# Optimization experiments

Measured on AMD Instinct MI355X. Metric: run time of the kernel, lower is better.

The kernel has to match this reference:

```python
import jax, jax.numpy as jnp
import numpy as np

N_NODES = 100000
N_EDGES = 3200000
F_IN, F_HID, F_OUT = 512, 16, 64


def gcn_conv(x, src, dst, W, b, n):
    # Linear transform first (PyG GCNConv: x @ W, then normalized aggregation, then + bias)
    xw = x @ W  # [n, f_out]
    # symmetric normalization with self-loops (gcn_norm, improved=False)
    deg = jax.ops.segment_sum(jnp.ones_like(dst, dtype=xw.dtype), dst, num_segments=n)
    deg_inv_sqrt = jnp.where(deg > 0, jax.lax.rsqrt(jnp.maximum(deg, 1e-12)), 0.0)
    norm = deg_inv_sqrt[src] * deg_inv_sqrt[dst]  # [E+n]
    out = jax.ops.segment_sum(norm[:, None] * xw[src], dst, num_segments=n)
    return out + b


def setup_inputs() -> dict:
    key = jax.random.key(0)
    k1, k2, k3, k4, k5, k6 = jax.random.split(key, 6)
    x = jax.random.normal(k1, (N_NODES, F_IN), dtype=jnp.float32)
    edge_index = jax.random.randint(k2, (2, N_EDGES), 0, N_NODES, dtype=jnp.int64)
    # Glorot init like PyG GCNConv
    s1 = (6.0 / (F_IN + F_HID)) ** 0.5
    s2 = (6.0 / (F_HID + F_OUT)) ** 0.5
    W1 = jax.random.uniform(k3, (F_IN, F_HID), jnp.float32, -s1, s1)
    b1 = jnp.zeros((F_HID,), jnp.float32)
    W2 = jax.random.uniform(k4, (F_HID, F_OUT), jnp.float32, -s2, s2)
    b2 = jnp.zeros((F_OUT,), jnp.float32)
    return {"x": x, "edge_index": edge_index, "W1": W1, "b1": b1, "W2": W2, "b2": b2}


def reference(x, edge_index, W1, b1, W2, b2):
    n = x.shape[0]
    loop = jnp.arange(n, dtype=edge_index.dtype)
    src = jnp.concatenate([edge_index[0], loop])
    dst = jnp.concatenate([edge_index[1], loop])
    h = jax.nn.relu(gcn_conv(x, src, dst, W1, b1, n))
    out = jax.nn.relu(gcn_conv(h, src, dst, W2, b2, n))
    return out
```

## Files before the change

### kernel.cpp

```cpp
#include <hip/hip_runtime.h>

constexpr int NN   = 100000;
constexpr int NE   = 3200000;
constexpr int FIN  = 512;
constexpr int FH   = 16;
constexpr int FOUT = 64;

constexpr int BSH = 6;
constexpr int BSZ = 64;
constexpr int K   = (NN + BSZ - 1) / BSZ;
constexpr int NB  = 512;
constexpr int CHUNK = NE / NB;
constexpr int CAP = 4096;

constexpr int G1B = 1024;
constexpr int G1T = 128;
constexpr int NPB = 98;

__global__ __launch_bounds__(256) void k_cnt(const int* __restrict__ ei, int* __restrict__ M) {
    __shared__ int h[K];
    int t = threadIdx.x, b = blockIdx.x;
    for (int i = t; i < K; i += 256) h[i] = 0;
    __syncthreads();
    int e0 = b * CHUNK, eend = e0 + CHUNK;
    int e = e0 + 4 * t;
    for (; e + 4 <= eend; e += 1024) {
        int d0 = ei[NE + e],     d1 = ei[NE + e + 1];
        int d2 = ei[NE + e + 2], d3 = ei[NE + e + 3];
        atomicAdd(&h[d0 >> BSH], 1);
        atomicAdd(&h[d1 >> BSH], 1);
        atomicAdd(&h[d2 >> BSH], 1);
        atomicAdd(&h[d3 >> BSH], 1);
    }
    for (int ee = e; ee < eend && ee < e + 4; ++ee)
        atomicAdd(&h[ei[NE + ee] >> BSH], 1);
    __syncthreads();
    for (int i = t; i < K; i += 256) M[i * NB + b] = h[i];
}

__global__ __launch_bounds__(256) void k_scanM(int* __restrict__ M, int* __restrict__ btot) {
    int k = blockIdx.x, t = threadIdx.x;
    int2* row = (int2*)(M + (size_t)k * NB);
    int2 v = row[t];
    int s = v.x + v.y;
    int lane = t & 63, wid = t >> 6;
    int ps = s;
    #pragma unroll
    for (int off = 1; off < 64; off <<= 1) {
        int u = __shfl_up(ps, off, 64);
        if (lane >= off) ps += u;
    }
    __shared__ int wsum[4];
    if (lane == 63) wsum[wid] = ps;
    __syncthreads();
    int base = 0;
    for (int w = 0; w < wid; ++w) base += wsum[w];
    int excl = base + ps - s;
    int2 o; o.x = excl; o.y = excl + v.x;
    row[t] = o;
    if (t == 255) btot[k] = excl + s;
}

__global__ __launch_bounds__(1024) void k_scanB(const int* __restrict__ btot, int* __restrict__ bstart) {
    int t = threadIdx.x;
    int i0 = 2 * t, i1 = 2 * t + 1;
    int c0 = (i0 < K) ? btot[i0] : 0;
    int c1 = (i1 < K) ? btot[i1] : 0;
    int s = c0 + c1;
    int lane = t & 63, wid = t >> 6;
    int ps = s;
    #pragma unroll
    for (int off = 1; off < 64; off <<= 1) {
        int u = __shfl_up(ps, off, 64);
        if (lane >= off) ps += u;
    }
    __shared__ int wsum[16];
    if (lane == 63) wsum[wid] = ps;
    __syncthreads();
    int base = 0;
    for (int w = 0; w < wid; ++w) base += wsum[w];
    int excl = base + ps - s;
    if (i0 < K) bstart[i0] = excl;
    if (i1 < K) bstart[i1] = excl + c0;
    if (t == 0) bstart[K] = NE;
}

__global__ __launch_bounds__(256) void k_scatter2(const int* __restrict__ ei,
                                                  const int* __restrict__ M,
                                                  const int* __restrict__ bstart,
                                                  int* __restrict__ rec) {
    __shared__ int cur[K];
    int t = threadIdx.x, b = blockIdx.x;
    for (int i = t; i < K; i += 256) cur[i] = bstart[i] + M[i * NB + b];
    __syncthreads();
    int e0 = b * CHUNK, eend = e0 + CHUNK;
    int e = e0 + 4 * t;
    for (; e + 4 <= eend; e += 1024) {
        int s0 = ei[e],     s1 = ei[e + 1],     s2 = ei[e + 2],     s3 = ei[e + 3];
        int d0 = ei[NE + e], d1 = ei[NE + e + 1], d2 = ei[NE + e + 2], d3 = ei[NE + e + 3];
        int p0 = atomicAdd(&cur[d0 >> BSH], 1);
        int p1 = atomicAdd(&cur[d1 >> BSH], 1);
        int p2 = atomicAdd(&cur[d2 >> BSH], 1);
        int p3 = atomicAdd(&cur[d3 >> BSH], 1);
        rec[p0] = (s0 << BSH) | (d0 & (BSZ - 1));
        rec[p1] = (s1 << BSH) | (d1 & (BSZ - 1));
        rec[p2] = (s2 << BSH) | (d2 & (BSZ - 1));
        rec[p3] = (s3 << BSH) | (d3 & (BSZ - 1));
    }
    for (int ee = e; ee < eend && ee < e + 4; ++ee) {
        int s = ei[ee];
        int d = ei[NE + ee];
        int pos = atomicAdd(&cur[d >> BSH], 1);
        rec[pos] = (s << BSH) | (d & (BSZ - 1));
    }
}

__global__ __launch_bounds__(256) void k_sort2(const int* __restrict__ rec1,
                                               const int* __restrict__ bstart,
                                               int* __restrict__ rec2,
                                               int* __restrict__ row_ptr,
                                               float* __restrict__ dis) {
    __shared__ int h[BSZ];
    __shared__ int cur[BSZ];
    int t = threadIdx.x, k = blockIdx.x;
    if (t < BSZ) h[t] = 0;
    __syncthreads();
    int e0 = bstart[k], e1 = bstart[k + 1];
    {
        int e = e0 + 4 * t;
        for (; e + 4 <= e1; e += 1024) {
            int r0 = rec1[e], r1 = rec1[e + 1], r2 = rec1[e + 2], r3 = rec1[e + 3];
            atomicAdd(&h[r0 & (BSZ - 1)], 1);
            atomicAdd(&h[r1 & (BSZ - 1)], 1);
            atomicAdd(&h[r2 & (BSZ - 1)], 1);
            atomicAdd(&h[r3 & (BSZ - 1)], 1);
        }
        for (int ee = e; ee < e1 && ee < e + 4; ++ee)
            atomicAdd(&h[rec1[ee] & (BSZ - 1)], 1);
    }
    __syncthreads();
    if (t < BSZ) {
        int c = h[t];
        int ps = c;
        #pragma unroll
        for (int off = 1; off < 64; off <<= 1) {
            int u = __shfl_up(ps, off, 64);
            if (t >= off) ps += u;
        }
        int excl = ps - c;
        cur[t] = excl;
        int node = k * BSZ + t;
        if (node < NN) {
            row_ptr[node] = e0 + excl;
            dis[node] = rsqrtf((float)c + 1.0f);
        }
    }
    __syncthreads();
    {
        int e = e0 + 4 * t;
        for (; e + 4 <= e1; e += 1024) {
            int r0 = rec1[e], r1 = rec1[e + 1], r2 = rec1[e + 2], r3 = rec1[e + 3];
            int p0 = atomicAdd(&cur[r0 & (BSZ - 1)], 1);
            int p1 = atomicAdd(&cur[r1 & (BSZ - 1)], 1);
            int p2 = atomicAdd(&cur[r2 & (BSZ - 1)], 1);
            int p3 = atomicAdd(&cur[r3 & (BSZ - 1)], 1);
            rec2[e0 + p0] = r0 >> BSH;
            rec2[e0 + p1] = r1 >> BSH;
            rec2[e0 + p2] = r2 >> BSH;
            rec2[e0 + p3] = r3 >> BSH;
        }
        for (int ee = e; ee < e1 && ee < e + 4; ++ee) {
            int r = rec1[ee];
            int pos = atomicAdd(&cur[r & (BSZ - 1)], 1);
            rec2[e0 + pos] = r >> BSH;
        }
    }
    if (k == 0 && t == 0) row_ptr[NN] = NE;
}

__device__ __forceinline__ void cons16(float acc[FH], float4 a0, float4 a1, float4 a2, float4 a3,
                                       const float* __restrict__ wrow) {
    float xs[16] = {a0.x, a0.y, a0.z, a0.w, a1.x, a1.y, a1.z, a1.w,
                    a2.x, a2.y, a2.z, a2.w, a3.x, a3.y, a3.z, a3.w};
    #pragma unroll
    for (int c = 0; c < 16; ++c) {
        float xv = xs[c];
        const float* w = &wrow[c * FH];
        #pragma unroll
        for (int jb = 0; jb < 4; ++jb) {
            float4 wv = *(const float4*)&w[jb * 4];
            acc[jb * 4 + 0] += xv * wv.x;
            acc[jb * 4 + 1] += xv * wv.y;
            acc[jb * 4 + 2] += xv * wv.z;
            acc[jb * 4 + 3] += xv * wv.w;
        }
    }
}

__global__ __launch_bounds__(G1T) void k_gemm1(const float* __restrict__ x,
                                               const float* __restrict__ W1,
                                               const float* __restrict__ dis,
                                               float* __restrict__ vp1) {
    __shared__ float ws[FIN * FH];
    int t = threadIdx.x;
    #pragma unroll
    for (int i = 0; i < 16; ++i)
        *(float4*)&ws[i * 512 + t * 4] = *(const float4*)&W1[i * 512 + t * 4];
    int node = blockIdx.x * NPB + t;
    bool live = (t < NPB) && (node < NN);
    int n = live ? node : NN - 1;
    const float* xr = x + (size_t)n * FIN;
    float acc[FH];
    #pragma unroll
    for (int j = 0; j < FH; ++j) acc[j] = 0.f;
    float4 A0 = *(const float4*)&xr[0],  A1 = *(const float4*)&xr[4],
           A2 = *(const float4*)&xr[8],  A3 = *(const float4*)&xr[12];
    float4 B0 = *(const float4*)&xr[16], B1 = *(const float4*)&xr[20],
           B2 = *(const float4*)&xr[24], B3 = *(const float4*)&xr[28];
    __syncthreads();
    #pragma unroll 1
    for (int k0 = 0; k0 + 48 <= FIN; k0 += 32) {
        float4 C0 = *(const float4*)&xr[k0 + 32], C1 = *(const float4*)&xr[k0 + 36],
               C2 = *(const float4*)&xr[k0 + 40], C3 = *(const float4*)&xr[k0 + 44];
        cons16(acc, A0, A1, A2, A3, &ws[k0 * FH]);
        A0 = C0; A1 = C1; A2 = C2; A3 = C3;
        float4 D0 = *(const float4*)&xr[k0 + 48], D1 = *(const float4*)&xr[k0 + 52],
               D2 = *(const float4*)&xr[k0 + 56], D3 = *(const float4*)&xr[k0 + 60];
        cons16(acc, B0, B1, B2, B3, &ws[(k0 + 16) * FH]);
        B0 = D0; B1 = D1; B2 = D2; B3 = D3;
    }
    cons16(acc, A0, A1, A2, A3, &ws[(FIN - 32) * FH]);
    cons16(acc, B0, B1, B2, B3, &ws[(FIN - 16) * FH]);
    if (live) {
        float dv = dis[node];
        #pragma unroll
        for (int jb = 0; jb < 4; ++jb)
            *(float4*)&vp1[(size_t)node * FH + jb * 4] =
                make_float4(dv * acc[jb * 4], dv * acc[jb * 4 + 1],
                            dv * acc[jb * 4 + 2], dv * acc[jb * 4 + 3]);
    }
}

__device__ __forceinline__ float4 seg_gather(const int* __restrict__ recs,
                                             const int* __restrict__ gsrc,
                                             int a, int b, int nst,
                                             const float* __restrict__ vp, int q) {
    float4 acc = make_float4(0.f, 0.f, 0.f, 0.f);
    int blds = b < nst ? b : nst;
    int i = a;
    for (; i + 8 <= blds; i += 8) {
        int r0 = recs[i],     r1 = recs[i + 1], r2 = recs[i + 2], r3 = recs[i + 3];
        int r4 = recs[i + 4], r5 = recs[i + 5], r6 = recs[i + 6], r7 = recs[i + 7];
        float4 v0 = *(const float4*)&vp[(size_t)r0 * FH + q * 4];
        float4 v1 = *(const float4*)&vp[(size_t)r1 * FH + q * 4];
        float4 v2 = *(const float4*)&vp[(size_t)r2 * FH + q * 4];
        float4 v3 = *(const float4*)&vp[(size_t)r3 * FH + q * 4];
        float4 v4 = *(const float4*)&vp[(size_t)r4 * FH + q * 4];
        float4 v5 = *(const float4*)&vp[(size_t)r5 * FH + q * 4];
        float4 v6 = *(const float4*)&vp[(size_t)r6 * FH + q * 4];
        float4 v7 = *(const float4*)&vp[(size_t)r7 * FH + q * 4];
        acc.x += ((v0.x + v1.x) + (v2.x + v3.x)) + ((v4.x + v5.x) + (v6.x + v7.x));
        acc.y += ((v0.y + v1.y) + (v2.y + v3.y)) + ((v4.y + v5.y) + (v6.y + v7.y));
        acc.z += ((v0.z + v1.z) + (v2.z + v3.z)) + ((v4.z + v5.z) + (v6.z + v7.z));
        acc.w += ((v0.w + v1.w) + (v2.w + v3.w)) + ((v4.w + v5.w) + (v6.w + v7.w));
    }
    for (; i < blds; ++i) {
        int r0 = recs[i];
        float4 v0 = *(const float4*)&vp[(size_t)r0 * FH + q * 4];
        acc.x += v0.x; acc.y += v0.y; acc.z += v0.z; acc.w += v0.w;
    }
    for (int j = (a > nst ? a : nst); j < b; ++j) {
        int r0 = gsrc[j];
        float4 v0 = *(const float4*)&vp[(size_t)r0 * FH + q * 4];
        acc.x += v0.x; acc.y += v0.y; acc.z += v0.z; acc.w += v0.w;
    }
    return acc;
}

__global__ __launch_bounds__(256) void k_agg1(const int* __restrict__ rec2,
                                              const int* __restrict__ bstart,
                                              const int* __restrict__ row_ptr,
                                              const float* __restrict__ dis,
                                              const float* __restrict__ vp1,
                                              const float* __restrict__ b1,
                                              float* __restrict__ vp2) {
    __shared__ int recs[CAP];
    int t = threadIdx.x, k = blockIdx.x;
    int e0 = bstart[k], e1 = bstart[k + 1];
    int len = e1 - e0, nst = len < CAP ? len : CAP;
    for (int i = t; i < nst; i += 256) recs[i] = rec2[e0 + i];
    __syncthreads();
    int slot = t >> 2, q = t & 3;
    int node = k * BSZ + slot;
    if (node >= NN) return;
    int a = row_ptr[node] - e0;
    int b = row_ptr[node + 1] - e0;
    float4 acc = seg_gather(recs, rec2 + e0, a, b, nst, vp1, q);
    float dv = dis[node];
    float4 self = *(const float4*)&vp1[(size_t)node * FH + q * 4];
    float4 bb   = *(const float4*)&b1[q * 4];
    float4 o;
    o.x = dv * fmaxf(dv * (acc.x + self.x) + bb.x, 0.f);
    o.y = dv * fmaxf(dv * (acc.y + self.y) + bb.y, 0.f);
    o.z = dv * fmaxf(dv * (acc.z + self.z) + bb.z, 0.f);
    o.w = dv * fmaxf(dv * (acc.w + self.w) + bb.w, 0.f);
    *(float4*)&vp2[(size_t)node * FH + q * 4] = o;
}

__global__ __launch_bounds__(256) void k_agg2(const int* __restrict__ rec2,
                                              const int* __restrict__ bstart,
                                              const int* __restrict__ row_ptr,
                                              const float* __restrict__ dis,
                                              const float* __restrict__ vp2,
                                              const float* __restrict__ W2,
                                              const float* __restrict__ b2,
                                              float* __restrict__ out) {
    __shared__ int   recs[CAP];
    __shared__ float a16[BSZ * FH];
    __shared__ float ws[FH * FOUT];
    int t = threadIdx.x, k = blockIdx.x;
    *(float4*)&ws[t * 4] = *(const float4*)&W2[t * 4];
    int e0 = bstart[k], e1 = bstart[k + 1];
    int len = e1 - e0, nst = len < CAP ? len : CAP;
    for (int i = t; i < nst; i += 256) recs[i] = rec2[e0 + i];
    __syncthreads();
    int slot = t >> 2, q = t & 3;
    int node = k * BSZ + slot;
    float4 r = make_float4(0.f, 0.f, 0.f, 0.f);
    if (node < NN) {
        int a = row_ptr[node] - e0;
        int b = row_ptr[node + 1] - e0;
        float4 acc = seg_gather(recs, rec2 + e0, a, b, nst, vp2, q);
        float dv = dis[node];
        float4 self = *(const float4*)&vp2[(size_t)node * FH + q * 4];
        r.x = dv * (acc.x + self.x);
        r.y = dv * (acc.y + self.y);
        r.z = dv * (acc.z + self.z);
        r.w = dv * (acc.w + self.w);
    }
    *(float4*)&a16[slot * FH + q * 4] = r;
    __syncthreads();
    int j = t & 63;
    float bj = b2[j];
    float wreg[FH];
    #pragma unroll
    for (int kk = 0; kk < FH; ++kk) wreg[kk] = ws[kk * FOUT + j];
    for (int n = t >> 6; n < BSZ; n += 4) {
        int node2 = k * BSZ + n;
        if (node2 >= NN) break;
        const float* ar = &a16[n * FH];
        float s = 0.f;
        #pragma unroll
        for (int kk = 0; kk < FH; ++kk) s += ar[kk] * wreg[kk];
        out[(size_t)node2 * FOUT + j] = fmaxf(s + bj, 0.f);
    }
}

extern "C" void kernel_launch(void* const* d_in, const int* in_sizes, int n_in,
                              void* d_out, int out_size, void* d_ws, size_t ws_size,
                              hipStream_t stream) {
    const float* x  = (const float*)d_in[0];
    const int*   ei = (const int*)d_in[1];
    const float* W1 = (const float*)d_in[2];
    const float* b1 = (const float*)d_in[3];
    const float* W2 = (const float*)d_in[4];
    const float* b2 = (const float*)d_in[5];
    float* out = (float*)d_out;

    char* p = (char*)d_ws;
    int*   M       = (int*)p;    p += (size_t)K * NB * 4;
    int*   btot    = (int*)p;    p += 2048 * 4;
    int*   bstart  = (int*)p;    p += 2048 * 4;
    char*  bufA    = p;          p += (size_t)NE * 4;
    int*   rec2    = (int*)p;    p += (size_t)NE * 4;
    int*   row_ptr = (int*)p;    p += 100032 * 4;
    float* dis     = (float*)p;  p += 100032 * 4;

    int*   rec1 = (int*)bufA;
    float* vp1  = (float*)bufA;
    float* vp2  = (float*)(bufA + (size_t)NN * FH * 4);

    k_cnt     <<<NB, 256, 0, stream>>>(ei, M);
    k_scanM   <<<K, 256, 0, stream>>>(M, btot);
    k_scanB   <<<1, 1024, 0, stream>>>(btot, bstart);
    k_scatter2<<<NB, 256, 0, stream>>>(ei, M, bstart, rec1);
    k_sort2   <<<K, 256, 0, stream>>>(rec1, bstart, rec2, row_ptr, dis);

    k_gemm1   <<<G1B, G1T, 0, stream>>>(x, W1, dis, vp1);
    k_agg1    <<<K, 256, 0, stream>>>(rec2, bstart, row_ptr, dis, vp1, b1, vp2);
    k_agg2    <<<K, 256, 0, stream>>>(rec2, bstart, row_ptr, dis, vp2, W2, b2, out);
}
```

Baseline: 469.9 us.

## Cut binning blocks to 128 and drop LDS staging of edge records in aggregation

The edge-binning passes now use 128 blocks instead of 512, which shrinks the per-block histogram matrix, lets the column scan run as a single 64-lane wavefront without shared memory, and removes the tail-edge loops since the chunk divides evenly. The aggregation kernels stop copying each bucket's source records into a 16 KB shared buffer and read them straight from global memory. This removes a barrier and the LDS footprint, which should help occupancy. In exchange the binning passes have fewer blocks, so less parallelism and more shared-atomic contention per block, and the index reads in aggregation now come from cache or global memory.

```diff
diff --git a/kernel.cpp b/kernel.cpp
--- a/kernel.cpp
+++ b/kernel.cpp
@@ -9,9 +9,8 @@
 constexpr int BSH = 6;
 constexpr int BSZ = 64;
 constexpr int K   = (NN + BSZ - 1) / BSZ;
-constexpr int NB  = 512;
+constexpr int NB  = 128;
 constexpr int CHUNK = NE / NB;
-constexpr int CAP = 4096;
 
 constexpr int G1B = 1024;
 constexpr int G1T = 128;
@@ -23,8 +22,7 @@
     for (int i = t; i < K; i += 256) h[i] = 0;
     __syncthreads();
     int e0 = b * CHUNK, eend = e0 + CHUNK;
-    int e = e0 + 4 * t;
-    for (; e + 4 <= eend; e += 1024) {
+    for (int e = e0 + 4 * t; e + 4 <= eend; e += 1024) {
         int d0 = ei[NE + e],     d1 = ei[NE + e + 1];
         int d2 = ei[NE + e + 2], d3 = ei[NE + e + 3];
         atomicAdd(&h[d0 >> BSH], 1);
@@ -32,33 +30,25 @@
         atomicAdd(&h[d2 >> BSH], 1);
         atomicAdd(&h[d3 >> BSH], 1);
     }
-    for (int ee = e; ee < eend && ee < e + 4; ++ee)
-        atomicAdd(&h[ei[NE + ee] >> BSH], 1);
     __syncthreads();
     for (int i = t; i < K; i += 256) M[i * NB + b] = h[i];
 }
 
-__global__ __launch_bounds__(256) void k_scanM(int* __restrict__ M, int* __restrict__ btot) {
+__global__ __launch_bounds__(64) void k_scanM(int* __restrict__ M, int* __restrict__ btot) {
     int k = blockIdx.x, t = threadIdx.x;
     int2* row = (int2*)(M + (size_t)k * NB);
     int2 v = row[t];
     int s = v.x + v.y;
-    int lane = t & 63, wid = t >> 6;
     int ps = s;
     #pragma unroll
     for (int off = 1; off < 64; off <<= 1) {
         int u = __shfl_up(ps, off, 64);
-        if (lane >= off) ps += u;
-    }
-    __shared__ int wsum[4];
-    if (lane == 63) wsum[wid] = ps;
-    __syncthreads();
-    int base = 0;
-    for (int w = 0; w < wid; ++w) base += wsum[w];
-    int excl = base + ps - s;
+        if (t >= off) ps += u;
+    }
+    int excl = ps - s;
     int2 o; o.x = excl; o.y = excl + v.x;
     row[t] = o;
-    if (t == 255) btot[k] = excl + s;
+    if (t == 63) btot[k] = excl + s;
 }
 
 __global__ __launch_bounds__(1024) void k_scanB(const int* __restrict__ btot, int* __restrict__ bstart) {
@@ -94,9 +84,8 @@
     for (int i = t; i < K; i += 256) cur[i] = bstart[i] + M[i * NB + b];
     __syncthreads();
     int e0 = b * CHUNK, eend = e0 + CHUNK;
-    int e = e0 + 4 * t;
-    for (; e + 4 <= eend; e += 1024) {
-        int s0 = ei[e],     s1 = ei[e + 1],     s2 = ei[e + 2],     s3 = ei[e + 3];
+    for (int e = e0 + 4 * t; e + 4 <= eend; e += 1024) {
+        int s0 = ei[e],      s1 = ei[e + 1],      s2 = ei[e + 2],      s3 = ei[e + 3];
         int d0 = ei[NE + e], d1 = ei[NE + e + 1], d2 = ei[NE + e + 2], d3 = ei[NE + e + 3];
         int p0 = atomicAdd(&cur[d0 >> BSH], 1);
         int p1 = atomicAdd(&cur[d1 >> BSH], 1);
@@ -106,12 +95,6 @@
         rec[p1] = (s1 << BSH) | (d1 & (BSZ - 1));
         rec[p2] = (s2 << BSH) | (d2 & (BSZ - 1));
         rec[p3] = (s3 << BSH) | (d3 & (BSZ - 1));
-    }
-    for (int ee = e; ee < eend && ee < e + 4; ++ee) {
-        int s = ei[ee];
-        int d = ei[NE + ee];
-        int pos = atomicAdd(&cur[d >> BSH], 1);
-        rec[pos] = (s << BSH) | (d & (BSZ - 1));
     }
 }
 
@@ -241,16 +224,14 @@
     }
 }
 
-__device__ __forceinline__ float4 seg_gather(const int* __restrict__ recs,
-                                             const int* __restrict__ gsrc,
-                                             int a, int b, int nst,
+__device__ __forceinline__ float4 seg_gather(const int* __restrict__ gsrc,
+                                             int a, int b,
                                              const float* __restrict__ vp, int q) {
     float4 acc = make_float4(0.f, 0.f, 0.f, 0.f);
-    int blds = b < nst ? b : nst;
     int i = a;
-    for (; i + 8 <= blds; i += 8) {
-        int r0 = recs[i],     r1 = recs[i + 1], r2 = recs[i + 2], r3 = recs[i + 3];
-        int r4 = recs[i + 4], r5 = recs[i + 5], r6 = recs[i + 6], r7 = recs[i + 7];
+    for (; i + 8 <= b; i += 8) {
+        int r0 = gsrc[i],     r1 = gsrc[i + 1], r2 = gsrc[i + 2], r3 = gsrc[i + 3];
+        int r4 = gsrc[i + 4], r5 = gsrc[i + 5], r6 = gsrc[i + 6], r7 = gsrc[i + 7];
         float4 v0 = *(const float4*)&vp[(size_t)r0 * FH + q * 4];
         float4 v1 = *(const float4*)&vp[(size_t)r1 * FH + q * 4];
         float4 v2 = *(const float4*)&vp[(size_t)r2 * FH + q * 4];
@@ -264,38 +245,27 @@
         acc.z += ((v0.z + v1.z) + (v2.z + v3.z)) + ((v4.z + v5.z) + (v6.z + v7.z));
         acc.w += ((v0.w + v1.w) + (v2.w + v3.w)) + ((v4.w + v5.w) + (v6.w + v7.w));
     }
-    for (; i < blds; ++i) {
-        int r0 = recs[i];
+    for (; i < b; ++i) {
+        int r0 = gsrc[i];
         float4 v0 = *(const float4*)&vp[(size_t)r0 * FH + q * 4];
         acc.x += v0.x; acc.y += v0.y; acc.z += v0.z; acc.w += v0.w;
     }
-    for (int j = (a > nst ? a : nst); j < b; ++j) {
-        int r0 = gsrc[j];
-        float4 v0 = *(const float4*)&vp[(size_t)r0 * FH + q * 4];
-        acc.x += v0.x; acc.y += v0.y; acc.z += v0.z; acc.w += v0.w;
-    }
     return acc;
 }
 
 __global__ __launch_bounds__(256) void k_agg1(const int* __restrict__ rec2,
-                                              const int* __restrict__ bstart,
                                               const int* __restrict__ row_ptr,
                                               const float* __restrict__ dis,
                                               const float* __restrict__ vp1,
                                               const float* __restrict__ b1,
                                               float* __restrict__ vp2) {
-    __shared__ int recs[CAP];
     int t = threadIdx.x, k = blockIdx.x;
-    int e0 = bstart[k], e1 = bstart[k + 1];
-    int len = e1 - e0, nst = len < CAP ? len : CAP;
-    for (int i = t; i < nst; i += 256) recs[i] = rec2[e0 + i];
-    __syncthreads();
     int slot = t >> 2, q = t & 3;
     int node = k * BSZ + slot;
     if (node >= NN) return;
-    int a = row_ptr[node] - e0;
-    int b = row_ptr[node + 1] - e0;
-    float4 acc = seg_gather(recs, rec2 + e0, a, b, nst, vp1, q);
+    int a = row_ptr[node];
+    int b = row_ptr[node + 1];
+    float4 acc = seg_gather(rec2, a, b, vp1, q);
     float dv = dis[node];
     float4 self = *(const float4*)&vp1[(size_t)node * FH + q * 4];
     float4 bb   = *(const float4*)&b1[q * 4];
@@ -308,29 +278,23 @@
 }
 
 __global__ __launch_bounds__(256) void k_agg2(const int* __restrict__ rec2,
-                                              const int* __restrict__ bstart,
                                               const int* __restrict__ row_ptr,
                                               const float* __restrict__ dis,
                                               const float* __restrict__ vp2,
                                               const float* __restrict__ W2,
                                               const float* __restrict__ b2,
                                               float* __restrict__ out) {
-    __shared__ int   recs[CAP];
     __shared__ float a16[BSZ * FH];
     __shared__ float ws[FH * FOUT];
     int t = threadIdx.x, k = blockIdx.x;
     *(float4*)&ws[t * 4] = *(const float4*)&W2[t * 4];
-    int e0 = bstart[k], e1 = bstart[k + 1];
-    int len = e1 - e0, nst = len < CAP ? len : CAP;
-    for (int i = t; i < nst; i += 256) recs[i] = rec2[e0 + i];
-    __syncthreads();
     int slot = t >> 2, q = t & 3;
     int node = k * BSZ + slot;
     float4 r = make_float4(0.f, 0.f, 0.f, 0.f);
     if (node < NN) {
-        int a = row_ptr[node] - e0;
-        int b = row_ptr[node + 1] - e0;
-        float4 acc = seg_gather(recs, rec2 + e0, a, b, nst, vp2, q);
+        int a = row_ptr[node];
+        int b = row_ptr[node + 1];
+        float4 acc = seg_gather(rec2, a, b, vp2, q);
         float dv = dis[node];
         float4 self = *(const float4*)&vp2[(size_t)node * FH + q * 4];
         r.x = dv * (acc.x + self.x);
@@ -381,12 +345,12 @@
     float* vp2  = (float*)(bufA + (size_t)NN * FH * 4);
 
     k_cnt     <<<NB, 256, 0, stream>>>(ei, M);
-    k_scanM   <<<K, 256, 0, stream>>>(M, btot);
+    k_scanM   <<<K, 64, 0, stream>>>(M, btot);
     k_scanB   <<<1, 1024, 0, stream>>>(btot, bstart);
     k_scatter2<<<NB, 256, 0, stream>>>(ei, M, bstart, rec1);
     k_sort2   <<<K, 256, 0, stream>>>(rec1, bstart, rec2, row_ptr, dis);
 
     k_gemm1   <<<G1B, G1T, 0, stream>>>(x, W1, dis, vp1);
-    k_agg1    <<<K, 256, 0, stream>>>(rec2, bstart, row_ptr, dis, vp1, b1, vp2);
-    k_agg2    <<<K, 256, 0, stream>>>(rec2, bstart, row_ptr, dis, vp2, W2, b2, out);
-}
+    k_agg1    <<<K, 256, 0, stream>>>(rec2, row_ptr, dis, vp1, b1, vp2);
+    k_agg2    <<<K, 256, 0, stream>>>(rec2, row_ptr, dis, vp2, W2, b2, out);
+}
```

Result: slower. 511.1 us (+8.8%).
